# Performance work log

Measured on AMD Instinct MI355X. Metric: run time of the kernel, lower is better.

Reference implementation:

```python
import jax, jax.numpy as jnp
import numpy as np

B, S, D, H, DFF = 4, 1024, 1024, 16, 4096
DK = D // H
EPS = 1e-9


def _layernorm(x, alpha, bias):
    # Faithful to source: torch.std is unbiased (ddof=1), eps added to std.
    mean = jnp.mean(x, axis=-1, keepdims=True)
    xc = x - mean
    std = jnp.sqrt(jnp.sum(xc * xc, axis=-1, keepdims=True) / (x.shape[-1] - 1))
    return alpha * xc / (std + EPS) + bias


def _mha(x, wq_w, wq_b, wo_w, wo_b):
    # Source bug preserved: w_q is used for q, k, AND v projections.
    p = (x @ wq_w + wq_b).reshape(B, S, H, DK).transpose(0, 2, 1, 3)  # [B,H,S,DK]
    scores = jnp.einsum('bhqd,bhkd->bhqk', p, p) / jnp.sqrt(jnp.asarray(DK, x.dtype))
    attn = jax.nn.softmax(scores, axis=-1)
    out = jnp.einsum('bhqk,bhkd->bhqd', attn, p)
    out = out.transpose(0, 2, 1, 3).reshape(B, S, D)
    return out @ wo_w + wo_b


def _ffn(x, w1, b1, w2, b2):
    return jax.nn.relu(x @ w1 + b1) @ w2 + b2


def setup_inputs() -> dict:
    key = jax.random.key(0)
    ks = jax.random.split(key, 8)
    sc = 0.02
    return {
        'x': jax.random.normal(ks[0], (B, S, D), jnp.float32),
        'wq_w': sc * jax.random.normal(ks[1], (D, D), jnp.float32),
        'wq_b': jnp.zeros((D,), jnp.float32),
        'wo_w': sc * jax.random.normal(ks[2], (D, D), jnp.float32),
        'wo_b': jnp.zeros((D,), jnp.float32),
        'ff1_w': sc * jax.random.normal(ks[3], (D, DFF), jnp.float32),
        'ff1_b': jnp.zeros((DFF,), jnp.float32),
        'ff2_w': sc * jax.random.normal(ks[4], (DFF, D), jnp.float32),
        'ff2_b': jnp.zeros((D,), jnp.float32),
        'alpha1': jnp.ones((1,), jnp.float32), 'bias1': jnp.zeros((1,), jnp.float32),
        'alpha2': jnp.ones((1,), jnp.float32), 'bias2': jnp.zeros((1,), jnp.float32),
        'alpha3': jnp.ones((1,), jnp.float32), 'bias3': jnp.zeros((1,), jnp.float32),
    }


def reference(x, wq_w, wq_b, wo_w, wo_b, ff1_w, ff1_b, ff2_w, ff2_b,
              alpha1, bias1, alpha2, bias2, alpha3, bias3):
    h1 = x + _mha(_layernorm(x, alpha1, bias1), wq_w, wq_b, wo_w, wo_b)
    h2 = h1 + _ffn(_layernorm(h1, alpha2, bias2), ff1_w, ff1_b, ff2_w, ff2_b)
    return _layernorm(h2, alpha3, bias3)
```

## Files before the change

kernel.cpp:

```cpp
#include <hip/hip_runtime.h>

typedef short short8 __attribute__((ext_vector_type(8)));
typedef float f32x4 __attribute__((ext_vector_type(4)));
typedef unsigned short u16x4 __attribute__((ext_vector_type(4)));

#define DEV static __device__ __forceinline__

DEV float b2f(unsigned short u) { return __uint_as_float(((unsigned)u) << 16); }
DEV unsigned short f2b(float f) {
    unsigned u = __float_as_uint(f);
    u += 0x7FFFu + ((u >> 16) & 1u);
    return (unsigned short)(u >> 16);
}
DEV float wred_sum(float v) {
#pragma unroll
    for (int o = 32; o; o >>= 1) v += __shfl_xor(v, o);
    return v;
}

DEV void gld_lds16(const unsigned short* g, unsigned short* l) {
    __builtin_amdgcn_global_load_lds((const __attribute__((address_space(1))) void*)g,
                                     (__attribute__((address_space(3))) void*)l, 16, 0, 0);
}

template <bool OUT_BF16>
__global__ __launch_bounds__(256) void ln_kernel(const float* __restrict__ in,
                                                 void* __restrict__ out_v,
                                                 const float* __restrict__ alpha_p,
                                                 const float* __restrict__ bias_p) {
    __shared__ float redA[4], redB[4];
    const int row = blockIdx.x;
    const int t = threadIdx.x;
    const int lane = t & 63, w = t >> 6;

    f32x4 xv = *(const f32x4*)&in[(size_t)row * 1024 + t * 4];

    float s = wred_sum(xv[0] + xv[1] + xv[2] + xv[3]);
    if (lane == 0) redA[w] = s;
    __syncthreads();
    float mean = (redA[0] + redA[1] + redA[2] + redA[3]) * (1.0f / 1024.0f);

    float d0 = xv[0] - mean, d1 = xv[1] - mean, d2 = xv[2] - mean, d3 = xv[3] - mean;
    float ss = wred_sum(d0 * d0 + d1 * d1 + d2 * d2 + d3 * d3);
    if (lane == 0) redB[w] = ss;
    __syncthreads();
    float var = (redB[0] + redB[1] + redB[2] + redB[3]) * (1.0f / 1023.0f);
    float denom = sqrtf(var) + 1e-9f;
    float inv = alpha_p[0] / denom;
    float bias = bias_p[0];

    if (OUT_BF16) {
        u16x4 o;
        o[0] = f2b(d0 * inv + bias);
        o[1] = f2b(d1 * inv + bias);
        o[2] = f2b(d2 * inv + bias);
        o[3] = f2b(d3 * inv + bias);
        *(u16x4*)&((unsigned short*)out_v)[(size_t)row * 1024 + t * 4] = o;
    } else {
        f32x4 o;
        o[0] = d0 * inv + bias;
        o[1] = d1 * inv + bias;
        o[2] = d2 * inv + bias;
        o[3] = d3 * inv + bias;
        *(f32x4*)&((float*)out_v)[(size_t)row * 1024 + t * 4] = o;
    }
}

__global__ __launch_bounds__(256) void prelude_kernel(
    const float* __restrict__ x, unsigned short* __restrict__ lnbuf,
    const float* __restrict__ alpha1, const float* __restrict__ bias1,
    const float* __restrict__ wq_w, unsigned short* __restrict__ wq_t,
    const float* __restrict__ wo_w, unsigned short* __restrict__ wo_t,
    const float* __restrict__ ff1_w, unsigned short* __restrict__ ff1_t,
    const float* __restrict__ ff2_w, unsigned short* __restrict__ ff2_t) {
    __shared__ unsigned short tile[32][33];
    __shared__ float redA[4], redB[4];
    const int t = threadIdx.x;
    int bid = blockIdx.x;

    if (bid < 4096) {
        const int row = bid;
        const int lane = t & 63, w = t >> 6;
        f32x4 xv = *(const f32x4*)&x[(size_t)row * 1024 + t * 4];
        float s = wred_sum(xv[0] + xv[1] + xv[2] + xv[3]);
        if (lane == 0) redA[w] = s;
        __syncthreads();
        float mean = (redA[0] + redA[1] + redA[2] + redA[3]) * (1.0f / 1024.0f);
        float d0 = xv[0] - mean, d1 = xv[1] - mean, d2 = xv[2] - mean, d3 = xv[3] - mean;
        float ss = wred_sum(d0 * d0 + d1 * d1 + d2 * d2 + d3 * d3);
        if (lane == 0) redB[w] = ss;
        __syncthreads();
        float var = (redB[0] + redB[1] + redB[2] + redB[3]) * (1.0f / 1023.0f);
        float inv = alpha1[0] / (sqrtf(var) + 1e-9f);
        float bias = bias1[0];
        u16x4 o;
        o[0] = f2b(d0 * inv + bias);
        o[1] = f2b(d1 * inv + bias);
        o[2] = f2b(d2 * inv + bias);
        o[3] = f2b(d3 * inv + bias);
        *(u16x4*)&lnbuf[(size_t)row * 1024 + t * 4] = o;
        return;
    }
    bid -= 4096;
    const float* src;
    unsigned short* dst;
    int R, C, gx;
    if (bid < 1024) {
        src = wq_w; dst = wq_t; R = 1024; C = 1024; gx = 32;
    } else if (bid < 2048) {
        bid -= 1024; src = wo_w; dst = wo_t; R = 1024; C = 1024; gx = 32;
    } else if (bid < 6144) {
        bid -= 2048; src = ff1_w; dst = ff1_t; R = 1024; C = 4096; gx = 128;
    } else {
        bid -= 6144; src = ff2_w; dst = ff2_t; R = 4096; C = 1024; gx = 32;
    }
    const int c0 = (bid % gx) * 32, r0 = (bid / gx) * 32;
    const int xx = t & 31, y0 = t >> 5;
#pragma unroll
    for (int yy = y0; yy < 32; yy += 8) tile[yy][xx] = f2b(src[(size_t)(r0 + yy) * C + c0 + xx]);
    __syncthreads();
#pragma unroll
    for (int yy = y0; yy < 32; yy += 8) dst[(size_t)(c0 + yy) * R + r0 + xx] = tile[xx][yy];
}

__global__ __launch_bounds__(256) void transpose_bf16_batch(const unsigned short* __restrict__ in,
                                                            unsigned short* __restrict__ out) {
    __shared__ unsigned short tile[32][33];
    const int b = blockIdx.z;
    const int d0 = blockIdx.x * 32, s0 = blockIdx.y * 32;
    const unsigned short* I = in + (size_t)b * 1024 * 1024;
    unsigned short* O = out + (size_t)b * 1024 * 1024;
    const int x = threadIdx.x, y0 = threadIdx.y;
#pragma unroll
    for (int yy = y0; yy < 32; yy += 8) tile[yy][x] = I[(size_t)(s0 + yy) * 1024 + d0 + x];
    __syncthreads();
#pragma unroll
    for (int yy = y0; yy < 32; yy += 8) O[(size_t)(d0 + yy) * 1024 + s0 + x] = tile[x][yy];
}

template <int BM, int BN, bool RELU, bool RES, bool OUT_BF16>
__global__ __launch_bounds__(256) void gemm2b(const unsigned short* __restrict__ A,
                                              const unsigned short* __restrict__ Bt,
                                              const float* __restrict__ bias,
                                              const float* __restrict__ res,
                                              void* __restrict__ C_v,
                                              int M, int N, int K) {
    constexpr int WM = BM / 2, WN = BN / 2;
    constexpr int FM = WM / 16, FN = WN / 16;
    __shared__ __align__(16) unsigned short As[3][BM * 64];
    __shared__ __align__(16) unsigned short Bs[3][BN * 64];

    const int t = threadIdx.x;
    const int lane = t & 63, w = t >> 6;
    const int wr = w >> 1, wc = w & 1;
    const int lr = lane & 15, g = lane >> 4;

    const int nwg = gridDim.x;
    const int cpx = nwg >> 3;
    const int wg = blockIdx.x;
    const int swz = (wg & 7) * cpx + (wg >> 3);
    const int NB = N / BN;
    const int m0 = (swz / NB) * BM, n0 = (swz % NB) * BN;

    f32x4 acc[FM][FN];
#pragma unroll
    for (int i = 0; i < FM; ++i)
#pragma unroll
        for (int j = 0; j < FN; ++j) acc[i][j] = (f32x4)0.0f;

    const int NT = K / 64;

#define STAGE2B(kt)                                                                        \
    {                                                                                      \
        const int buf_ = (kt) % 3;                                                         \
        const int k0_ = (kt) * 64;                                                         \
        _Pragma("unroll") for (int i = 0; i < BM / 32; ++i) {                              \
            int id = i * 256 + t;                                                          \
            int row = id >> 3, ch = (id & 7) ^ (row & 7);                                  \
            gld_lds16(&A[(size_t)(m0 + row) * K + k0_ + ch * 8],                           \
                      &As[buf_][(size_t)(i * 256 + (t & ~63)) * 8]);                       \
        }                                                                                  \
        _Pragma("unroll") for (int i = 0; i < BN / 32; ++i) {                              \
            int id = i * 256 + t;                                                          \
            int row = id >> 3, ch = (id & 7) ^ (row & 7);                                  \
            gld_lds16(&Bt[(size_t)(n0 + row) * K + k0_ + ch * 8],                          \
                      &Bs[buf_][(size_t)(i * 256 + (t & ~63)) * 8]);                       \
        }                                                                                  \
    }

    STAGE2B(0);
    STAGE2B(1);
    asm volatile("s_waitcnt vmcnt(6)" ::: "memory");
    __builtin_amdgcn_sched_barrier(0);
    __builtin_amdgcn_s_barrier();

    for (int kt = 0; kt < NT; ++kt) {
        const int buf = kt % 3;
        if (kt + 2 < NT) STAGE2B(kt + 2);

        short8 af[FM][2], bfr[FN][2];
#pragma unroll
        for (int mi = 0; mi < FM; ++mi) {
            int row = wr * WM + mi * 16 + lr;
#pragma unroll
            for (int ks = 0; ks < 2; ++ks) {
                int ch = (ks * 4 + g) ^ (row & 7);
                af[mi][ks] = *(const short8*)&As[buf][row * 64 + ch * 8];
            }
        }
#pragma unroll
        for (int ni = 0; ni < FN; ++ni) {
            int row = wc * WN + ni * 16 + lr;
#pragma unroll
            for (int ks = 0; ks < 2; ++ks) {
                int ch = (ks * 4 + g) ^ (row & 7);
                bfr[ni][ks] = *(const short8*)&Bs[buf][row * 64 + ch * 8];
            }
        }

        __builtin_amdgcn_s_setprio(1);
#pragma unroll
        for (int ks = 0; ks < 2; ++ks)
#pragma unroll
            for (int mi = 0; mi < FM; ++mi)
#pragma unroll
                for (int ni = 0; ni < FN; ++ni)
                    acc[mi][ni] = __builtin_amdgcn_mfma_f32_16x16x32_bf16(af[mi][ks], bfr[ni][ks], acc[mi][ni], 0, 0, 0);
        __builtin_amdgcn_s_setprio(0);

        if (kt + 2 < NT) {
            asm volatile("s_waitcnt vmcnt(6)" ::: "memory");
        } else if (kt + 1 < NT) {
            asm volatile("s_waitcnt vmcnt(0)" ::: "memory");
        }
        __builtin_amdgcn_sched_barrier(0);
        __builtin_amdgcn_s_barrier();
    }
#undef STAGE2B

    const int lg = g;
#pragma unroll
    for (int ni = 0; ni < FN; ++ni) {
        int col = n0 + wc * WN + ni * 16 + lr;
        float bv = bias[col];
#pragma unroll
        for (int mi = 0; mi < FM; ++mi) {
            int row0 = m0 + wr * WM + mi * 16 + lg * 4;
#pragma unroll
            for (int i = 0; i < 4; ++i) {
                int row = row0 + i;
                float x = acc[mi][ni][i] + bv;
                if (RES) x += res[(size_t)row * N + col];
                if (RELU) x = fmaxf(x, 0.0f);
                if (OUT_BF16)
                    ((unsigned short*)C_v)[(size_t)row * N + col] = f2b(x);
                else
                    ((float*)C_v)[(size_t)row * N + col] = x;
            }
        }
    }
}

template <bool RELU, bool OUT_BF16>
__global__ __launch_bounds__(512, 4) void gemm3b(const unsigned short* __restrict__ A,
                                                 const unsigned short* __restrict__ Bt,
                                                 const float* __restrict__ bias,
                                                 void* __restrict__ C_v,
                                                 int M, int N, int K) {
    __shared__ __align__(16) unsigned short As[3][256 * 32];
    __shared__ __align__(16) unsigned short Bs[3][128 * 32];

    const int t = threadIdx.x;
    const int lane = t & 63;
    const int wid = t >> 6;
    const int wr = wid >> 1, wc = wid & 1;
    const int lr = lane & 15, g = lane >> 4;

    const int nwg = gridDim.x;
    const int cpx = nwg >> 3;
    const int wg = blockIdx.x;
    const int swz = (wg & 7) * cpx + (wg >> 3);
    const int NB = N / 128;
    const int m0 = (swz / NB) * 256, n0 = (swz % NB) * 128;

    f32x4 acc[4][4];
#pragma unroll
    for (int i = 0; i < 4; ++i)
#pragma unroll
        for (int j = 0; j < 4; ++j) acc[i][j] = (f32x4)0.0f;

    const int NT = K / 32;

#define STAGE3B(kt)                                                                         \
    {                                                                                       \
        const int buf_ = (kt) % 3;                                                          \
        const int k0_ = (kt) * 32;                                                          \
        _Pragma("unroll") for (int s = 0; s < 2; ++s) {                                     \
            int id = s * 512 + t;                                                           \
            int row = id >> 2;                                                              \
            int ch = (id & 3) ^ ((row >> 1) & 3);                                           \
            gld_lds16(&A[(size_t)(m0 + row) * K + k0_ + ch * 8],                            \
                      &As[buf_][(size_t)(s * 512 + (t & ~63)) * 8]);                        \
        }                                                                                   \
        {                                                                                   \
            int row = t >> 2;                                                               \
            int ch = (t & 3) ^ ((row >> 1) & 3);                                            \
            gld_lds16(&Bt[(size_t)(n0 + row) * K + k0_ + ch * 8],                           \
                      &Bs[buf_][(size_t)(t & ~63) * 8]);                                    \
        }                                                                                   \
    }

    STAGE3B(0);
    STAGE3B(1);
    asm volatile("s_waitcnt vmcnt(3)" ::: "memory");
    __builtin_amdgcn_sched_barrier(0);
    __builtin_amdgcn_s_barrier();

    for (int kt = 0; kt < NT; ++kt) {
        const int buf = kt % 3;
        if (kt + 2 < NT) STAGE3B(kt + 2);

        short8 af[4], bf[4];
#pragma unroll
        for (int mi = 0; mi < 4; ++mi) {
            int row = wr * 64 + mi * 16 + lr;
            int ch = g ^ ((row >> 1) & 3);
            af[mi] = *(const short8*)&As[buf][row * 32 + ch * 8];
        }
#pragma unroll
        for (int nj = 0; nj < 4; ++nj) {
            int row = wc * 64 + nj * 16 + lr;
            int ch = g ^ ((row >> 1) & 3);
            bf[nj] = *(const short8*)&Bs[buf][row * 32 + ch * 8];
        }

        __builtin_amdgcn_s_setprio(1);
#pragma unroll
        for (int mi = 0; mi < 4; ++mi)
#pragma unroll
            for (int nj = 0; nj < 4; ++nj)
                acc[mi][nj] = __builtin_amdgcn_mfma_f32_16x16x32_bf16(af[mi], bf[nj], acc[mi][nj], 0, 0, 0);
        __builtin_amdgcn_s_setprio(0);

        if (kt + 2 < NT) {
            asm volatile("s_waitcnt vmcnt(3)" ::: "memory");
        } else if (kt + 1 < NT) {
            asm volatile("s_waitcnt vmcnt(0)" ::: "memory");
        }
        __builtin_amdgcn_sched_barrier(0);
        __builtin_amdgcn_s_barrier();
    }
#undef STAGE3B

#pragma unroll
    for (int nj = 0; nj < 4; ++nj) {
        int col = n0 + wc * 64 + nj * 16 + lr;
        float bv = bias[col];
#pragma unroll
        for (int mi = 0; mi < 4; ++mi) {
            int row0 = m0 + wr * 64 + mi * 16 + g * 4;
#pragma unroll
            for (int i = 0; i < 4; ++i) {
                int row = row0 + i;
                float x = acc[mi][nj][i] + bv;
                if (RELU) x = fmaxf(x, 0.0f);
                if (OUT_BF16)
                    ((unsigned short*)C_v)[(size_t)row * N + col] = f2b(x);
                else
                    ((float*)C_v)[(size_t)row * N + col] = x;
            }
        }
    }
}

__global__ __launch_bounds__(256) void attn_mfma_kernel(const unsigned short* __restrict__ p,
                                                        const unsigned short* __restrict__ pT,
                                                        unsigned short* __restrict__ out) {
    __shared__ __align__(16) unsigned short Ks[64 * 64];
    __shared__ __align__(16) unsigned short Vt[64 * 64];
    __shared__ __align__(16) unsigned short Ps[4 * 16 * 64];

    const int t = threadIdx.x;
    const int lane = t & 63, w = t >> 6;
    const int lr = lane & 15, g = lane >> 4;
    const int bh = blockIdx.x;
    const int qblk = blockIdx.y;
    const int b = bh >> 4, h = bh & 15;

    const unsigned short* Pm = p + (size_t)b * (1024 * 1024) + h * 64;
    const unsigned short* PT = pT + (size_t)b * (1024 * 1024) + (size_t)(h * 64) * 1024;

    const int q0 = qblk * 64 + w * 16;
    short8 qa0 = *(const short8*)&Pm[(size_t)(q0 + lr) * 1024 + g * 8];
    short8 qa1 = *(const short8*)&Pm[(size_t)(q0 + lr) * 1024 + 32 + g * 8];

    f32x4 acc[4];
#pragma unroll
    for (int i = 0; i < 4; ++i) acc[i] = (f32x4)0.0f;
    float mrow[4] = {-1e30f, -1e30f, -1e30f, -1e30f};
    float lsum[4] = {0.f, 0.f, 0.f, 0.f};

    unsigned short* Pw = &Ps[w * 16 * 64];

    for (int kt = 0; kt < 16; ++kt) {
        const int key0 = kt * 64;
        __syncthreads();
#pragma unroll
        for (int i = 0; i < 2; ++i) {
            int id = t + i * 256;
            int row = id >> 3, ch = (id & 7) * 8;
            int sw = ch ^ ((row & 7) << 3);
            short8 kv = *(const short8*)&Pm[(size_t)(key0 + row) * 1024 + ch];
            *(short8*)&Ks[row * 64 + sw] = kv;
            short8 vv = *(const short8*)&PT[(size_t)row * 1024 + key0 + ch];
            *(short8*)&Vt[row * 64 + sw] = vv;
        }
        __syncthreads();

        f32x4 s_acc[4];
#pragma unroll
        for (int kg = 0; kg < 4; ++kg) {
            s_acc[kg] = (f32x4)0.0f;
            int krow = kg * 16 + lr;
            int swz = (krow & 7) << 3;
            short8 kb0 = *(const short8*)&Ks[krow * 64 + ((g * 8) ^ swz)];
            short8 kb1 = *(const short8*)&Ks[krow * 64 + ((32 + g * 8) ^ swz)];
            s_acc[kg] = __builtin_amdgcn_mfma_f32_16x16x32_bf16(qa0, kb0, s_acc[kg], 0, 0, 0);
            s_acc[kg] = __builtin_amdgcn_mfma_f32_16x16x32_bf16(qa1, kb1, s_acc[kg], 0, 0, 0);
        }

#pragma unroll
        for (int reg = 0; reg < 4; ++reg) {
            float mx = fmaxf(fmaxf(s_acc[0][reg], s_acc[1][reg]),
                             fmaxf(s_acc[2][reg], s_acc[3][reg])) * 0.125f;
            mx = fmaxf(mx, __shfl_xor(mx, 1));
            mx = fmaxf(mx, __shfl_xor(mx, 2));
            mx = fmaxf(mx, __shfl_xor(mx, 4));
            mx = fmaxf(mx, __shfl_xor(mx, 8));
            float mnew = fmaxf(mrow[reg], mx);
            float scale = __expf(mrow[reg] - mnew);
            mrow[reg] = mnew;
            float psum = 0.f;
#pragma unroll
            for (int kg = 0; kg < 4; ++kg) {
                float pv = __expf(s_acc[kg][reg] * 0.125f - mnew);
                s_acc[kg][reg] = pv;
                psum += pv;
            }
            psum += __shfl_xor(psum, 1);
            psum += __shfl_xor(psum, 2);
            psum += __shfl_xor(psum, 4);
            psum += __shfl_xor(psum, 8);
            lsum[reg] = lsum[reg] * scale + psum;
#pragma unroll
            for (int dg = 0; dg < 4; ++dg) acc[dg][reg] *= scale;
        }

#pragma unroll
        for (int reg = 0; reg < 4; ++reg) {
            int q = g * 4 + reg;
            int swz = (q & 7) << 3;
#pragma unroll
            for (int kg = 0; kg < 4; ++kg) {
                int key = lr + 16 * kg;
                Pw[q * 64 + (key ^ swz)] = f2b(s_acc[kg][reg]);
            }
        }
        int pswz = (lr & 7) << 3;
        short8 pa0 = *(const short8*)&Pw[lr * 64 + ((g * 8) ^ pswz)];
        short8 pa1 = *(const short8*)&Pw[lr * 64 + ((32 + g * 8) ^ pswz)];

#pragma unroll
        for (int dg = 0; dg < 4; ++dg) {
            int drow = dg * 16 + lr;
            int swz = (drow & 7) << 3;
            short8 vb0 = *(const short8*)&Vt[drow * 64 + ((g * 8) ^ swz)];
            short8 vb1 = *(const short8*)&Vt[drow * 64 + ((32 + g * 8) ^ swz)];
            acc[dg] = __builtin_amdgcn_mfma_f32_16x16x32_bf16(pa0, vb0, acc[dg], 0, 0, 0);
            acc[dg] = __builtin_amdgcn_mfma_f32_16x16x32_bf16(pa1, vb1, acc[dg], 0, 0, 0);
        }
    }

    unsigned short* O = out + (size_t)b * (1024 * 1024) + h * 64;
#pragma unroll
    for (int reg = 0; reg < 4; ++reg) {
        float inv = 1.0f / lsum[reg];
        int q = q0 + g * 4 + reg;
#pragma unroll
        for (int dg = 0; dg < 4; ++dg) {
            O[(size_t)q * 1024 + dg * 16 + lr] = f2b(acc[dg][reg] * inv);
        }
    }
}

extern "C" void kernel_launch(void* const* d_in, const int* in_sizes, int n_in,
                              void* d_out, int out_size, void* d_ws, size_t ws_size,
                              hipStream_t stream) {
    const float* x = (const float*)d_in[0];
    const float* wq_w = (const float*)d_in[1];
    const float* wq_b = (const float*)d_in[2];
    const float* wo_w = (const float*)d_in[3];
    const float* wo_b = (const float*)d_in[4];
    const float* ff1_w = (const float*)d_in[5];
    const float* ff1_b = (const float*)d_in[6];
    const float* ff2_w = (const float*)d_in[7];
    const float* ff2_b = (const float*)d_in[8];
    const float* alpha1 = (const float*)d_in[9];
    const float* bias1 = (const float*)d_in[10];
    const float* alpha2 = (const float*)d_in[11];
    const float* bias2 = (const float*)d_in[12];
    const float* alpha3 = (const float*)d_in[13];
    const float* bias3 = (const float*)d_in[14];
    float* out = (float*)d_out;

    const size_t MB = 1u << 20;
    char* ws = (char*)d_ws;
    unsigned short* wq_t = (unsigned short*)(ws + 0 * MB);
    unsigned short* wo_t = (unsigned short*)(ws + 2 * MB);
    unsigned short* ff1_t = (unsigned short*)(ws + 4 * MB);
    unsigned short* ff2_t = (unsigned short*)(ws + 12 * MB);
    unsigned short* lnbuf = (unsigned short*)(ws + 20 * MB);
    unsigned short* pbuf = (unsigned short*)(ws + 28 * MB);
    unsigned short* attn = (unsigned short*)(ws + 36 * MB);
    float* h1 = (float*)(ws + 44 * MB);
    unsigned short* pbT = (unsigned short*)(ws + 60 * MB);
    unsigned short* mid = (unsigned short*)(ws + 60 * MB);
    float* h2 = (float*)(ws + 28 * MB);

    const int M = 4096;

    prelude_kernel<<<14336, 256, 0, stream>>>(x, lnbuf, alpha1, bias1,
                                              wq_w, wq_t, wo_w, wo_t,
                                              ff1_w, ff1_t, ff2_w, ff2_t);
    gemm2b<128, 64, false, false, true><<<512, 256, 0, stream>>>(lnbuf, wq_t, wq_b, nullptr, pbuf, M, 1024, 1024);
    transpose_bf16_batch<<<dim3(32, 32, 4), dim3(32, 8), 0, stream>>>(pbuf, pbT);
    attn_mfma_kernel<<<dim3(64, 16), 256, 0, stream>>>(pbuf, pbT, attn);
    gemm2b<128, 64, false, true, false><<<512, 256, 0, stream>>>(attn, wo_t, wo_b, x, h1, M, 1024, 1024);
    ln_kernel<true><<<M, 256, 0, stream>>>(h1, lnbuf, alpha2, bias2);
    gemm3b<true, true><<<512, 512, 0, stream>>>(lnbuf, ff1_t, ff1_b, mid, M, 4096, 1024);
    gemm2b<128, 64, false, true, false><<<512, 256, 0, stream>>>(mid, ff2_t, ff2_b, h1, h2, M, 1024, 4096);
    ln_kernel<false><<<M, 256, 0, stream>>>(h2, out, alpha3, bias3);
}
```

Baseline: 233.0 us.

## Fuse P transpose into QKV GEMM epilogue and store residuals as bf16

The projection GEMM epilogue now also writes the per-batch transposed copy of P directly, which removes the separate transpose kernel launch and its extra read pass over P. The residual streams h1 and h2 become bf16 instead of fp32, roughly halving the traffic for the residual adds and the layernorm reads. The cost is lower precision in the residual path, which could affect numerical accuracy. The transposed stores are 4-element vectors at a 2KB stride and may coalesce poorly.

```diff
diff --git a/kernel.cpp b/kernel.cpp
--- a/kernel.cpp
+++ b/kernel.cpp
@@ -23,8 +23,8 @@
                                      (__attribute__((address_space(3))) void*)l, 16, 0, 0);
 }
 
-template <bool OUT_BF16>
-__global__ __launch_bounds__(256) void ln_kernel(const float* __restrict__ in,
+template <bool IN_BF16, bool OUT_BF16>
+__global__ __launch_bounds__(256) void ln_kernel(const void* __restrict__ in_v,
                                                  void* __restrict__ out_v,
                                                  const float* __restrict__ alpha_p,
                                                  const float* __restrict__ bias_p) {
@@ -33,14 +33,21 @@
     const int t = threadIdx.x;
     const int lane = t & 63, w = t >> 6;
 
-    f32x4 xv = *(const f32x4*)&in[(size_t)row * 1024 + t * 4];
-
-    float s = wred_sum(xv[0] + xv[1] + xv[2] + xv[3]);
+    float x0, x1, x2, x3;
+    if (IN_BF16) {
+        u16x4 raw = *(const u16x4*)&((const unsigned short*)in_v)[(size_t)row * 1024 + t * 4];
+        x0 = b2f(raw[0]); x1 = b2f(raw[1]); x2 = b2f(raw[2]); x3 = b2f(raw[3]);
+    } else {
+        f32x4 xv = *(const f32x4*)&((const float*)in_v)[(size_t)row * 1024 + t * 4];
+        x0 = xv[0]; x1 = xv[1]; x2 = xv[2]; x3 = xv[3];
+    }
+
+    float s = wred_sum(x0 + x1 + x2 + x3);
     if (lane == 0) redA[w] = s;
     __syncthreads();
     float mean = (redA[0] + redA[1] + redA[2] + redA[3]) * (1.0f / 1024.0f);
 
-    float d0 = xv[0] - mean, d1 = xv[1] - mean, d2 = xv[2] - mean, d3 = xv[3] - mean;
+    float d0 = x0 - mean, d1 = x1 - mean, d2 = x2 - mean, d3 = x3 - mean;
     float ss = wred_sum(d0 * d0 + d1 * d1 + d2 * d2 + d3 * d3);
     if (lane == 0) redB[w] = ss;
     __syncthreads();
@@ -123,27 +130,13 @@
     for (int yy = y0; yy < 32; yy += 8) dst[(size_t)(c0 + yy) * R + r0 + xx] = tile[xx][yy];
 }
 
-__global__ __launch_bounds__(256) void transpose_bf16_batch(const unsigned short* __restrict__ in,
-                                                            unsigned short* __restrict__ out) {
-    __shared__ unsigned short tile[32][33];
-    const int b = blockIdx.z;
-    const int d0 = blockIdx.x * 32, s0 = blockIdx.y * 32;
-    const unsigned short* I = in + (size_t)b * 1024 * 1024;
-    unsigned short* O = out + (size_t)b * 1024 * 1024;
-    const int x = threadIdx.x, y0 = threadIdx.y;
-#pragma unroll
-    for (int yy = y0; yy < 32; yy += 8) tile[yy][x] = I[(size_t)(s0 + yy) * 1024 + d0 + x];
-    __syncthreads();
-#pragma unroll
-    for (int yy = y0; yy < 32; yy += 8) O[(size_t)(d0 + yy) * 1024 + s0 + x] = tile[x][yy];
-}
-
-template <int BM, int BN, bool RELU, bool RES, bool OUT_BF16>
+template <int BM, int BN, bool RELU, int RES_MODE, bool OUT_BF16, bool WRITE_T>
 __global__ __launch_bounds__(256) void gemm2b(const unsigned short* __restrict__ A,
                                               const unsigned short* __restrict__ Bt,
                                               const float* __restrict__ bias,
-                                              const float* __restrict__ res,
+                                              const void* __restrict__ res,
                                               void* __restrict__ C_v,
+                                              unsigned short* __restrict__ Ct,
                                               int M, int N, int K) {
     constexpr int WM = BM / 2, WN = BN / 2;
     constexpr int FM = WM / 16, FN = WN / 16;
@@ -246,16 +239,25 @@
 #pragma unroll
         for (int mi = 0; mi < FM; ++mi) {
             int row0 = m0 + wr * WM + mi * 16 + lg * 4;
+            u16x4 tv;
 #pragma unroll
             for (int i = 0; i < 4; ++i) {
                 int row = row0 + i;
                 float x = acc[mi][ni][i] + bv;
-                if (RES) x += res[(size_t)row * N + col];
+                if (RES_MODE == 1) x += ((const float*)res)[(size_t)row * N + col];
+                if (RES_MODE == 2) x += b2f(((const unsigned short*)res)[(size_t)row * N + col]);
                 if (RELU) x = fmaxf(x, 0.0f);
-                if (OUT_BF16)
-                    ((unsigned short*)C_v)[(size_t)row * N + col] = f2b(x);
-                else
+                if (OUT_BF16) {
+                    unsigned short v = f2b(x);
+                    ((unsigned short*)C_v)[(size_t)row * N + col] = v;
+                    if (WRITE_T) tv[i] = v;
+                } else {
                     ((float*)C_v)[(size_t)row * N + col] = x;
+                }
+            }
+            if (WRITE_T) {
+                int bb = row0 >> 10, s = row0 & 1023;
+                *(u16x4*)&Ct[(size_t)bb * (1024 * 1024) + (size_t)col * 1024 + s] = tv;
             }
         }
     }
@@ -522,22 +524,21 @@
     unsigned short* lnbuf = (unsigned short*)(ws + 20 * MB);
     unsigned short* pbuf = (unsigned short*)(ws + 28 * MB);
     unsigned short* attn = (unsigned short*)(ws + 36 * MB);
-    float* h1 = (float*)(ws + 44 * MB);
+    unsigned short* h1 = (unsigned short*)(ws + 44 * MB);
+    unsigned short* h2 = (unsigned short*)(ws + 52 * MB);
     unsigned short* pbT = (unsigned short*)(ws + 60 * MB);
     unsigned short* mid = (unsigned short*)(ws + 60 * MB);
-    float* h2 = (float*)(ws + 28 * MB);
 
     const int M = 4096;
 
     prelude_kernel<<<14336, 256, 0, stream>>>(x, lnbuf, alpha1, bias1,
                                               wq_w, wq_t, wo_w, wo_t,
                                               ff1_w, ff1_t, ff2_w, ff2_t);
-    gemm2b<128, 64, false, false, true><<<512, 256, 0, stream>>>(lnbuf, wq_t, wq_b, nullptr, pbuf, M, 1024, 1024);
-    transpose_bf16_batch<<<dim3(32, 32, 4), dim3(32, 8), 0, stream>>>(pbuf, pbT);
+    gemm2b<128, 64, false, 0, true, true><<<512, 256, 0, stream>>>(lnbuf, wq_t, wq_b, nullptr, pbuf, pbT, M, 1024, 1024);
     attn_mfma_kernel<<<dim3(64, 16), 256, 0, stream>>>(pbuf, pbT, attn);
-    gemm2b<128, 64, false, true, false><<<512, 256, 0, stream>>>(attn, wo_t, wo_b, x, h1, M, 1024, 1024);
-    ln_kernel<true><<<M, 256, 0, stream>>>(h1, lnbuf, alpha2, bias2);
+    gemm2b<128, 64, false, 1, true, false><<<512, 256, 0, stream>>>(attn, wo_t, wo_b, x, h1, nullptr, M, 1024, 1024);
+    ln_kernel<true, true><<<M, 256, 0, stream>>>(h1, lnbuf, alpha2, bias2);
     gemm3b<true, true><<<512, 512, 0, stream>>>(lnbuf, ff1_t, ff1_b, mid, M, 4096, 1024);
-    gemm2b<128, 64, false, true, false><<<512, 256, 0, stream>>>(mid, ff2_t, ff2_b, h1, h2, M, 1024, 4096);
-    ln_kernel<false><<<M, 256, 0, stream>>>(h2, out, alpha3, bias3);
-}
+    gemm2b<128, 64, false, 2, true, false><<<512, 256, 0, stream>>>(mid, ff2_t, ff2_b, h1, h2, nullptr, M, 1024, 4096);
+    ln_kernel<true, false><<<M, 256, 0, stream>>>(h2, out, alpha3, bias3);
+}
```

After: 226.4 us. 1.03x faster.
